# Optimization experiments

Measured on AMD Instinct MI355X. Metric: run time of the kernel, lower is better.

Reference implementation:

```python
import jax, jax.numpy as jnp
import numpy as np

COEFF = 0.95  # de-emphasis coefficient from __init__ default


def setup_inputs() -> dict:
    key = jax.random.key(0)
    # [batch, time] raw audio-like waveform
    x = jax.random.normal(key, (64, 524288), dtype=jnp.float32)
    return {"inputs": x}


def reference(inputs):
    """De-emphasis IIR filter: y[0] = x[0], y[n] = COEFF * y[n-1] + x[n].

    The original TF code runs a serial per-sample loop with tf.concat (O(T^2)).
    This is a first-order linear recurrence, expressed here as a log-depth
    associative scan over pairs (a, b) representing the affine map
    y -> a*y + b, with composition (a1,b1) then (a2,b2) = (a1*a2, a2*b1 + b2).
    Note a[0] never enters the output (only b of the first element does),
    so y[0] = x[0] exactly as in the original.
    """
    if COEFF <= 0:
        return inputs
    a = jnp.full(inputs.shape, COEFF, dtype=inputs.dtype)

    def combine(c1, c2):
        a1, b1 = c1
        a2, b2 = c2
        return (a1 * a2, a2 * b1 + b2)

    _, y = jax.lax.associative_scan(combine, (a, inputs), axis=1)
    return y
```

## Files before the change

kernel.cpp:

```cpp
#include <hip/hip_runtime.h>


#define T_LEN   524288
#define WCHUNK  2048
#define HALO    256
#define CPR     (T_LEN / WCHUNK)
#define L2C95   (-0.07400058f)
#define C32     (0.19371149f)

__global__ __launch_bounds__(256, 8)
void deemph_kernel(const float4* __restrict__ xin, float4* __restrict__ yout) {
    const int lane = threadIdx.x & 63;
    const int wv   = threadIdx.x >> 6;
    const int g    = blockIdx.x * 4 + wv;
    const int row  = g >> 8;
    const int ck   = g & (CPR - 1);

    const int row4   = row * (T_LEN / 4);
    const int cbase4 = ck * (WCHUNK / 4);
    const int base4  = row4 + cbase4;

    float IC = 0.f;
    if (ck != 0) {
        const float4 h = xin[base4 - (HALO / 4) + lane];
        float hl = h.x;
        hl = fmaf(0.95f, hl, h.y);
        hl = fmaf(0.95f, hl, h.z);
        hl = fmaf(0.95f, hl, h.w);
        float t = hl * exp2f((float)(4 * (63 - lane)) * L2C95);
        #pragma unroll
        for (int d = 1; d < 64; d <<= 1) t += __shfl_xor(t, d, 64);
        IC = t;
    }

    const float4* __restrict__ src = xin + base4 + lane * 8;
    float4 q[8];
    #pragma unroll
    for (int k = 0; k < 8; ++k) q[k] = src[k];

    float f = 0.f;
    #pragma unroll
    for (int k = 0; k < 8; ++k) {
        f = fmaf(0.95f, f, q[k].x);
        f = fmaf(0.95f, f, q[k].y);
        f = fmaf(0.95f, f, q[k].z);
        f = fmaf(0.95f, f, q[k].w);
    }

    float y = f;
    float m = C32;
    #pragma unroll
    for (int d = 1; d < 64; d <<= 1) {
        const float up = __shfl_up(y, d, 64);
        if (lane >= d) y = fmaf(m, up, y);
        m = m * m;
    }
    const float yup = __shfl_up(y, 1, 64);
    const float E = ((lane > 0) ? yup : 0.f)
                  + exp2f((float)(32 * lane) * L2C95) * IC;

    float4* __restrict__ dst = yout + base4 + lane * 8;
    float yy = E;
    #pragma unroll
    for (int k = 0; k < 8; ++k) {
        float4 v = q[k];
        yy = fmaf(0.95f, yy, v.x); v.x = yy;
        yy = fmaf(0.95f, yy, v.y); v.y = yy;
        yy = fmaf(0.95f, yy, v.z); v.z = yy;
        yy = fmaf(0.95f, yy, v.w); v.w = yy;
        dst[k] = v;
    }
}

extern "C" void kernel_launch(void* const* d_in, const int* in_sizes, int n_in,
                              void* d_out, int out_size, void* d_ws, size_t ws_size,
                              hipStream_t stream) {
    const float4* xin  = (const float4*)d_in[0];
    float4*       yout = (float4*)d_out;
    const int rows   = in_sizes[0] / T_LEN;
    const int waves  = rows * CPR;
    const int blocks = waves / 4;
    deemph_kernel<<<dim3(blocks), dim3(256), 0, stream>>>(xin, yout);
}
```

Measured before the change: 238.1 us.

## Switch to lane-interleaved coalesced float4 access with per-tile wave scans

Each lane now loads and stores float4s strided by 64 across the wave, so accesses are fully coalesced instead of each lane touching 8 contiguous float4s. The recurrence is computed as 8 sequential 256-sample tiles, each using a wave-wide shuffle scan, with a running carry Y passed between tiles. The halo prefix is also computed with a shuffle scan rather than a weighted reduction. This trades more shuffle and ALU work (9 scans instead of 1) for better memory access patterns, in a kernel that is memory-bound.

```diff
diff --git a/kernel.cpp b/kernel.cpp
--- a/kernel.cpp
+++ b/kernel.cpp
@@ -3,10 +3,11 @@
 
 #define T_LEN   524288
 #define WCHUNK  2048
-#define HALO    256
+#define NT      8
 #define CPR     (T_LEN / WCHUNK)
 #define L2C95   (-0.07400058f)
-#define C32     (0.19371149f)
+#define C4      (0.81450625f)
+#define C256    (1.9875265e-6f)
 
 __global__ __launch_bounds__(256, 8)
 void deemph_kernel(const float4* __restrict__ xin, float4* __restrict__ yout) {
@@ -16,59 +17,55 @@
     const int row  = g >> 8;
     const int ck   = g & (CPR - 1);
 
-    const int row4   = row * (T_LEN / 4);
-    const int cbase4 = ck * (WCHUNK / 4);
-    const int base4  = row4 + cbase4;
+    const int base4 = row * (T_LEN / 4) + ck * (WCHUNK / 4);
 
-    float IC = 0.f;
-    if (ck != 0) {
-        const float4 h = xin[base4 - (HALO / 4) + lane];
-        float hl = h.x;
-        hl = fmaf(0.95f, hl, h.y);
-        hl = fmaf(0.95f, hl, h.z);
-        hl = fmaf(0.95f, hl, h.w);
-        float t = hl * exp2f((float)(4 * (63 - lane)) * L2C95);
+    float4 h;
+    if (ck != 0) h = xin[base4 - 64 + lane];
+    else         h = make_float4(0.f, 0.f, 0.f, 0.f);
+    float4 q[NT];
+    #pragma unroll
+    for (int k = 0; k < NT; ++k) q[k] = xin[base4 + 64 * k + lane];
+
+    const float wl = exp2f((float)(4 * lane) * L2C95);
+
+    float Y;
+    {
+        float f = h.x;
+        f = fmaf(0.95f, f, h.y);
+        f = fmaf(0.95f, f, h.z);
+        f = fmaf(0.95f, f, h.w);
+        float y = f, m = C4;
         #pragma unroll
-        for (int d = 1; d < 64; d <<= 1) t += __shfl_xor(t, d, 64);
-        IC = t;
+        for (int d = 1; d < 64; d <<= 1) {
+            const float up = __shfl_up(y, d, 64);
+            if (lane >= d) y = fmaf(m, up, y);
+            m = m * m;
+        }
+        Y = __shfl(y, 63, 64);
     }
 
-    const float4* __restrict__ src = xin + base4 + lane * 8;
-    float4 q[8];
     #pragma unroll
-    for (int k = 0; k < 8; ++k) q[k] = src[k];
-
-    float f = 0.f;
-    #pragma unroll
-    for (int k = 0; k < 8; ++k) {
-        f = fmaf(0.95f, f, q[k].x);
-        f = fmaf(0.95f, f, q[k].y);
-        f = fmaf(0.95f, f, q[k].z);
-        f = fmaf(0.95f, f, q[k].w);
-    }
-
-    float y = f;
-    float m = C32;
-    #pragma unroll
-    for (int d = 1; d < 64; d <<= 1) {
-        const float up = __shfl_up(y, d, 64);
-        if (lane >= d) y = fmaf(m, up, y);
-        m = m * m;
-    }
-    const float yup = __shfl_up(y, 1, 64);
-    const float E = ((lane > 0) ? yup : 0.f)
-                  + exp2f((float)(32 * lane) * L2C95) * IC;
-
-    float4* __restrict__ dst = yout + base4 + lane * 8;
-    float yy = E;
-    #pragma unroll
-    for (int k = 0; k < 8; ++k) {
+    for (int k = 0; k < NT; ++k) {
         float4 v = q[k];
+        float f = v.x;
+        f = fmaf(0.95f, f, v.y);
+        f = fmaf(0.95f, f, v.z);
+        f = fmaf(0.95f, f, v.w);
+        float y = f, m = C4;
+        #pragma unroll
+        for (int d = 1; d < 64; d <<= 1) {
+            const float up = __shfl_up(y, d, 64);
+            if (lane >= d) y = fmaf(m, up, y);
+            m = m * m;
+        }
+        const float yup = __shfl_up(y, 1, 64);
+        float yy = ((lane > 0) ? yup : 0.f) + wl * Y;
         yy = fmaf(0.95f, yy, v.x); v.x = yy;
         yy = fmaf(0.95f, yy, v.y); v.y = yy;
         yy = fmaf(0.95f, yy, v.z); v.z = yy;
         yy = fmaf(0.95f, yy, v.w); v.w = yy;
-        dst[k] = v;
+        yout[base4 + 64 * k + lane] = v;
+        Y = fmaf(C256, Y, __shfl(y, 63, 64));
     }
 }
 
```

Result: faster. 228.7 us (-4.0%).
